# Optimization experiments

Hardware: AMD Instinct MI355X
Metric: run time of the kernel (lower is better)

The kernel has to match this reference:

```python
import jax, jax.numpy as jnp
import numpy as np

E = 3_200_000
D = 16
N = 100_000


def setup_inputs() -> dict:
    key = jax.random.key(0)
    k1, k2 = jax.random.split(key)
    x = jax.random.normal(k1, (E, D), dtype=jnp.float32)
    edge_dst = jax.random.randint(k2, (E,), 0, N, dtype=jnp.int64)
    return {"x": x, "edge_dst": edge_dst, "num_nodes": N}


def reference(x, edge_dst, num_nodes):
    # sum_over_neighbours: scatter-add edge features to destination atoms -> [N, D]
    summed = jax.ops.segment_sum(x, edge_dst, num_segments=num_nodes)
    # number_of_neighbours(include_central_atom=True): per-atom edge count + 1
    counts = jax.ops.segment_sum(
        jnp.ones((x.shape[0],), dtype=x.dtype), edge_dst, num_segments=num_nodes
    ) + jnp.asarray(1.0, dtype=x.dtype)
    # left_aligned_div by sqrt(counts): broadcast counts over trailing feature dims
    return summed / jnp.sqrt(counts)[:, None]
```

## Files before the change

### kernel.cpp

```cpp
#include <hip/hip_runtime.h>

#define DFEAT 16
#define NPB 64
#define NPB_SHIFT 6
#define EB 8192
#define EB_SHIFT 13
#define BIN_THREADS 1024
#define SCAN_BLOCKS 256
#define SCAN_THREADS 256
#define SORT_CAP 4096

__global__ void na_bin_kernel(const int* __restrict__ edge_dst,
                              unsigned short* __restrict__ rank,
                              int* __restrict__ hist,
                              int E, int B, int nblocks) {
    extern __shared__ int h[];
    const int b = blockIdx.x;
    const int t = threadIdx.x;
    for (int i = t; i < B; i += BIN_THREADS) h[i] = 0;
    __syncthreads();
    const int base = b * EB;
    #pragma unroll
    for (int j = 0; j < EB / BIN_THREADS; ++j) {
        int e = base + j * BIN_THREADS + t;
        if (e < E) {
            int k = edge_dst[e] >> NPB_SHIFT;
            int r = atomicAdd(&h[k], 1);
            rank[e] = (unsigned short)r;
        }
    }
    __syncthreads();
    for (int i = t; i < B; i += BIN_THREADS)
        hist[(size_t)i * nblocks + b] = h[i];
}

__global__ void na_scan_partials(const int* __restrict__ data,
                                 int* __restrict__ blockSums, int M) {
    __shared__ int lds[SCAN_THREADS];
    const int b = blockIdx.x, t = threadIdx.x;
    const int chb = (M + SCAN_BLOCKS - 1) / SCAN_BLOCKS;
    const int bbeg = b * chb;
    const int bend = min(bbeg + chb, M);
    const int cht = (chb + SCAN_THREADS - 1) / SCAN_THREADS;
    const int beg = min(bbeg + t * cht, bend);
    const int end = min(beg + cht, bend);
    int s = 0;
    for (int i = beg; i < end; ++i) s += data[i];
    lds[t] = s;
    __syncthreads();
    for (int off = SCAN_THREADS / 2; off > 0; off >>= 1) {
        if (t < off) lds[t] += lds[t + off];
        __syncthreads();
    }
    if (t == 0) blockSums[b] = lds[0];
}

__global__ void na_scan_blocksums(const int* __restrict__ blockSums,
                                  int* __restrict__ blockOffs) {
    __shared__ int lds[SCAN_BLOCKS];
    const int t = threadIdx.x;
    int v = blockSums[t];
    lds[t] = v;
    __syncthreads();
    for (int off = 1; off < SCAN_BLOCKS; off <<= 1) {
        int add = (t >= off) ? lds[t - off] : 0;
        __syncthreads();
        lds[t] += add;
        __syncthreads();
    }
    blockOffs[t] = lds[t] - v;
}

__global__ void na_scan_final(int* __restrict__ data,
                              const int* __restrict__ blockOffs, int M) {
    __shared__ int lds[SCAN_THREADS];
    const int b = blockIdx.x, t = threadIdx.x;
    const int chb = (M + SCAN_BLOCKS - 1) / SCAN_BLOCKS;
    const int bbeg = b * chb;
    const int bend = min(bbeg + chb, M);
    const int cht = (chb + SCAN_THREADS - 1) / SCAN_THREADS;
    const int beg = min(bbeg + t * cht, bend);
    const int end = min(beg + cht, bend);
    int s = 0;
    for (int i = beg; i < end; ++i) s += data[i];
    lds[t] = s;
    __syncthreads();
    for (int off = 1; off < SCAN_THREADS; off <<= 1) {
        int add = (t >= off) ? lds[t - off] : 0;
        __syncthreads();
        lds[t] += add;
        __syncthreads();
    }
    int run = blockOffs[b] + lds[t] - s;
    for (int i = beg; i < end; ++i) {
        int c = data[i];
        data[i] = run;
        run += c;
    }
}

__global__ void na_scatter_bin(const int* __restrict__ edge_dst,
                               const unsigned short* __restrict__ rank,
                               const int* __restrict__ offs,
                               int* __restrict__ binned,
                               int E, int nblocks) {
    int e = blockIdx.x * blockDim.x + threadIdx.x;
    if (e >= E) return;
    int n = edge_dst[e];
    int k = n >> NPB_SHIFT;
    int b = e >> EB_SHIFT;
    int pos = offs[(size_t)k * nblocks + b] + (int)rank[e];
    binned[pos] = ((n & (NPB - 1)) << 22) | e;
}

__global__ __launch_bounds__(256, 4)
void na_sort_gather(const float* __restrict__ x,
                    const int* __restrict__ binned,
                    const int* __restrict__ offs,
                    float* __restrict__ out,
                    int E, int N, int B, int nblocks) {
    __shared__ int buf[SORT_CAP];
    __shared__ int sorted[SORT_CAP];
    __shared__ int cnt[NPB];
    __shared__ int cur[NPB];
    __shared__ int excl[NPB + 1];

    const int k = blockIdx.x;
    const int t = threadIdx.x;

    const int beg = offs[(size_t)k * nblocks];
    const int end = (k + 1 < B) ? offs[(size_t)(k + 1) * nblocks] : E;
    const int sz = end - beg;

    if (t < NPB) { cnt[t] = 0; cur[t] = 0; }
    __syncthreads();

    if (sz <= SORT_CAP) {
        for (int j = t; j < sz; j += 256) {
            int v = binned[beg + j];
            buf[j] = v;
            atomicAdd(&cnt[v >> 22], 1);
        }
        __syncthreads();
        if (t == 0) {
            int run = 0;
            for (int d = 0; d < NPB; ++d) { excl[d] = run; run += cnt[d]; }
            excl[NPB] = run;
        }
        __syncthreads();
        for (int j = t; j < sz; j += 256) {
            int v = buf[j];
            int d = v >> 22;
            int r = atomicAdd(&cur[d], 1);
            sorted[excl[d] + r] = v & 0x3FFFFF;
        }
        __syncthreads();

        const int g = t >> 4;
        const int lane16 = t & 15;
        const int es = lane16 >> 2;
        const int q = lane16 & 3;
        const float4* x4 = reinterpret_cast<const float4*>(x);

        for (int ln = g; ln < NPB; ln += 16) {
            int n = k * NPB + ln;
            if (n >= N) break;
            int lbeg = excl[ln], lend = excl[ln + 1];
            float ax = 0.f, ay = 0.f, az = 0.f, aw = 0.f;

            int i = lbeg + es;
            for (; i + 12 < lend; i += 16) {
                int e0 = sorted[i];
                int e1 = sorted[i + 4];
                int e2 = sorted[i + 8];
                int e3 = sorted[i + 12];
                float4 v0 = x4[(size_t)e0 * 4 + q];
                float4 v1 = x4[(size_t)e1 * 4 + q];
                float4 v2 = x4[(size_t)e2 * 4 + q];
                float4 v3 = x4[(size_t)e3 * 4 + q];
                ax += (v0.x + v1.x) + (v2.x + v3.x);
                ay += (v0.y + v1.y) + (v2.y + v3.y);
                az += (v0.z + v1.z) + (v2.z + v3.z);
                aw += (v0.w + v1.w) + (v2.w + v3.w);
            }
            for (; i < lend; i += 4) {
                int e0 = sorted[i];
                float4 v0 = x4[(size_t)e0 * 4 + q];
                ax += v0.x; ay += v0.y; az += v0.z; aw += v0.w;
            }

            ax += __shfl_xor(ax, 4); ay += __shfl_xor(ay, 4);
            az += __shfl_xor(az, 4); aw += __shfl_xor(aw, 4);
            ax += __shfl_xor(ax, 8); ay += __shfl_xor(ay, 8);
            az += __shfl_xor(az, 8); aw += __shfl_xor(aw, 8);

            float s = rsqrtf((float)(lend - lbeg) + 1.0f);
            if (es == 0) {
                float4 r; r.x = ax * s; r.y = ay * s; r.z = az * s; r.w = aw * s;
                reinterpret_cast<float4*>(out)[(size_t)n * 4 + q] = r;
            }
        }
    } else {
        const int g = t >> 4;
        const int f = t & 15;
        for (int ln = g; ln < NPB; ln += 16) {
            int n = k * NPB + ln;
            if (n >= N) break;
            float acc = 0.0f;
            int deg = 0;
            for (int j = 0; j < sz; ++j) {
                int v = binned[beg + j];
                if ((v >> 22) == ln) {
                    acc += x[(size_t)(v & 0x3FFFFF) * DFEAT + f];
                    ++deg;
                }
            }
            out[(size_t)n * DFEAT + f] = acc * rsqrtf((float)deg + 1.0f);
        }
    }
}

extern "C" void kernel_launch(void* const* d_in, const int* in_sizes, int n_in,
                              void* d_out, int out_size, void* d_ws, size_t ws_size,
                              hipStream_t stream) {
    const float* x        = (const float*)d_in[0];
    const int*   edge_dst = (const int*)d_in[1];
    float*       out      = (float*)d_out;

    const int E = in_sizes[1];
    const int N = out_size / DFEAT;
    const int B = (N + NPB - 1) >> NPB_SHIFT;
    const int nblocks = (E + EB - 1) >> EB_SHIFT;
    const int M = B * nblocks;

    unsigned short* rank = (unsigned short*)d_ws;
    int* binned    = (int*)((char*)d_ws + (((size_t)E * 2 + 3) & ~(size_t)3));
    int* hist      = binned + E;
    int* blockSums = hist + M;
    int* blockOffs = blockSums + SCAN_BLOCKS;

    na_bin_kernel<<<nblocks, BIN_THREADS, B * sizeof(int), stream>>>(
        edge_dst, rank, hist, E, B, nblocks);
    na_scan_partials<<<SCAN_BLOCKS, SCAN_THREADS, 0, stream>>>(hist, blockSums, M);
    na_scan_blocksums<<<1, SCAN_BLOCKS, 0, stream>>>(blockSums, blockOffs);
    na_scan_final<<<SCAN_BLOCKS, SCAN_THREADS, 0, stream>>>(hist, blockOffs, M);
    na_scatter_bin<<<(E + 255) / 256, 256, 0, stream>>>(
        edge_dst, rank, hist, binned, E, nblocks);
    na_sort_gather<<<B, 256, 0, stream>>>(x, binned, hist, out, E, N, B, nblocks);
}
```

Baseline: 125.5 us.

## Drop rank array by recomputing bin positions with LDS atomics in scatter

The histogram kernel no longer writes a per-edge 16-bit rank. Instead the scatter kernel loads each block's scanned offsets into shared memory and takes positions with LDS atomics, which removes the rank write and read traffic. The gather stage now assigns one node per 4-thread group with an 8-way unrolled edge loop and no cross-lane shuffle reduction, and the serial 64-entry prefix sum becomes a wavefront shuffle scan. The edge order within a bin becomes nondeterministic, so floating-point summation order can vary from run to run, and load balance across threads now follows node degree.

```diff
diff --git a/kernel.cpp b/kernel.cpp
--- a/kernel.cpp
+++ b/kernel.cpp
@@ -11,7 +11,6 @@
 #define SORT_CAP 4096
 
 __global__ void na_bin_kernel(const int* __restrict__ edge_dst,
-                              unsigned short* __restrict__ rank,
                               int* __restrict__ hist,
                               int E, int B, int nblocks) {
     extern __shared__ int h[];
@@ -23,11 +22,7 @@
     #pragma unroll
     for (int j = 0; j < EB / BIN_THREADS; ++j) {
         int e = base + j * BIN_THREADS + t;
-        if (e < E) {
-            int k = edge_dst[e] >> NPB_SHIFT;
-            int r = atomicAdd(&h[k], 1);
-            rank[e] = (unsigned short)r;
-        }
+        if (e < E) atomicAdd(&h[edge_dst[e] >> NPB_SHIFT], 1);
     }
     __syncthreads();
     for (int i = t; i < B; i += BIN_THREADS)
@@ -99,18 +94,26 @@
     }
 }
 
-__global__ void na_scatter_bin(const int* __restrict__ edge_dst,
-                               const unsigned short* __restrict__ rank,
-                               const int* __restrict__ offs,
-                               int* __restrict__ binned,
-                               int E, int nblocks) {
-    int e = blockIdx.x * blockDim.x + threadIdx.x;
-    if (e >= E) return;
-    int n = edge_dst[e];
-    int k = n >> NPB_SHIFT;
-    int b = e >> EB_SHIFT;
-    int pos = offs[(size_t)k * nblocks + b] + (int)rank[e];
-    binned[pos] = ((n & (NPB - 1)) << 22) | e;
+__global__ void na_scatter_fused(const int* __restrict__ edge_dst,
+                                 const int* __restrict__ offs,
+                                 int* __restrict__ binned,
+                                 int E, int B, int nblocks) {
+    extern __shared__ int h[];
+    const int b = blockIdx.x;
+    const int t = threadIdx.x;
+    for (int i = t; i < B; i += BIN_THREADS)
+        h[i] = offs[(size_t)i * nblocks + b];
+    __syncthreads();
+    const int base = b * EB;
+    #pragma unroll
+    for (int j = 0; j < EB / BIN_THREADS; ++j) {
+        int e = base + j * BIN_THREADS + t;
+        if (e < E) {
+            int n = edge_dst[e];
+            int pos = atomicAdd(&h[n >> NPB_SHIFT], 1);
+            binned[pos] = ((n & (NPB - 1)) << 22) | e;
+        }
+    }
 }
 
 __global__ __launch_bounds__(256, 4)
@@ -142,10 +145,16 @@
             atomicAdd(&cnt[v >> 22], 1);
         }
         __syncthreads();
-        if (t == 0) {
-            int run = 0;
-            for (int d = 0; d < NPB; ++d) { excl[d] = run; run += cnt[d]; }
-            excl[NPB] = run;
+        if (t < 64) {
+            int v = cnt[t];
+            int inc = v;
+            #pragma unroll
+            for (int d = 1; d < 64; d <<= 1) {
+                int u = __shfl_up(inc, d);
+                if (t >= d) inc += u;
+            }
+            excl[t] = inc - v;
+            if (t == 63) excl[NPB] = inc;
         }
         __syncthreads();
         for (int j = t; j < sz; j += 256) {
@@ -156,66 +165,63 @@
         }
         __syncthreads();
 
-        const int g = t >> 4;
-        const int lane16 = t & 15;
-        const int es = lane16 >> 2;
-        const int q = lane16 & 3;
+        const int ln = t >> 2;
+        const int q = t & 3;
         const float4* x4 = reinterpret_cast<const float4*>(x);
 
-        for (int ln = g; ln < NPB; ln += 16) {
-            int n = k * NPB + ln;
-            if (n >= N) break;
-            int lbeg = excl[ln], lend = excl[ln + 1];
+        const int lbeg = excl[ln], lend = excl[ln + 1];
+        float ax = 0.f, ay = 0.f, az = 0.f, aw = 0.f;
+
+        int i = lbeg;
+        for (; i + 8 <= lend; i += 8) {
+            int e0 = sorted[i + 0], e1 = sorted[i + 1];
+            int e2 = sorted[i + 2], e3 = sorted[i + 3];
+            int e4 = sorted[i + 4], e5 = sorted[i + 5];
+            int e6 = sorted[i + 6], e7 = sorted[i + 7];
+            float4 v0 = x4[(size_t)e0 * 4 + q];
+            float4 v1 = x4[(size_t)e1 * 4 + q];
+            float4 v2 = x4[(size_t)e2 * 4 + q];
+            float4 v3 = x4[(size_t)e3 * 4 + q];
+            float4 v4 = x4[(size_t)e4 * 4 + q];
+            float4 v5 = x4[(size_t)e5 * 4 + q];
+            float4 v6 = x4[(size_t)e6 * 4 + q];
+            float4 v7 = x4[(size_t)e7 * 4 + q];
+            ax += ((v0.x + v1.x) + (v2.x + v3.x)) + ((v4.x + v5.x) + (v6.x + v7.x));
+            ay += ((v0.y + v1.y) + (v2.y + v3.y)) + ((v4.y + v5.y) + (v6.y + v7.y));
+            az += ((v0.z + v1.z) + (v2.z + v3.z)) + ((v4.z + v5.z) + (v6.z + v7.z));
+            aw += ((v0.w + v1.w) + (v2.w + v3.w)) + ((v4.w + v5.w) + (v6.w + v7.w));
+        }
+        for (; i < lend; ++i) {
+            int e0 = sorted[i];
+            float4 v0 = x4[(size_t)e0 * 4 + q];
+            ax += v0.x; ay += v0.y; az += v0.z; aw += v0.w;
+        }
+
+        int n = k * NPB + ln;
+        if (n < N) {
+            float s = rsqrtf((float)(lend - lbeg) + 1.0f);
+            float4 r; r.x = ax * s; r.y = ay * s; r.z = az * s; r.w = aw * s;
+            reinterpret_cast<float4*>(out)[(size_t)n * 4 + q] = r;
+        }
+    } else {
+        const int ln = t >> 2;
+        const int q = t & 3;
+        const float4* x4 = reinterpret_cast<const float4*>(x);
+        int n = k * NPB + ln;
+        if (n < N) {
             float ax = 0.f, ay = 0.f, az = 0.f, aw = 0.f;
-
-            int i = lbeg + es;
-            for (; i + 12 < lend; i += 16) {
-                int e0 = sorted[i];
-                int e1 = sorted[i + 4];
-                int e2 = sorted[i + 8];
-                int e3 = sorted[i + 12];
-                float4 v0 = x4[(size_t)e0 * 4 + q];
-                float4 v1 = x4[(size_t)e1 * 4 + q];
-                float4 v2 = x4[(size_t)e2 * 4 + q];
-                float4 v3 = x4[(size_t)e3 * 4 + q];
-                ax += (v0.x + v1.x) + (v2.x + v3.x);
-                ay += (v0.y + v1.y) + (v2.y + v3.y);
-                az += (v0.z + v1.z) + (v2.z + v3.z);
-                aw += (v0.w + v1.w) + (v2.w + v3.w);
-            }
-            for (; i < lend; i += 4) {
-                int e0 = sorted[i];
-                float4 v0 = x4[(size_t)e0 * 4 + q];
-                ax += v0.x; ay += v0.y; az += v0.z; aw += v0.w;
-            }
-
-            ax += __shfl_xor(ax, 4); ay += __shfl_xor(ay, 4);
-            az += __shfl_xor(az, 4); aw += __shfl_xor(aw, 4);
-            ax += __shfl_xor(ax, 8); ay += __shfl_xor(ay, 8);
-            az += __shfl_xor(az, 8); aw += __shfl_xor(aw, 8);
-
-            float s = rsqrtf((float)(lend - lbeg) + 1.0f);
-            if (es == 0) {
-                float4 r; r.x = ax * s; r.y = ay * s; r.z = az * s; r.w = aw * s;
-                reinterpret_cast<float4*>(out)[(size_t)n * 4 + q] = r;
-            }
-        }
-    } else {
-        const int g = t >> 4;
-        const int f = t & 15;
-        for (int ln = g; ln < NPB; ln += 16) {
-            int n = k * NPB + ln;
-            if (n >= N) break;
-            float acc = 0.0f;
             int deg = 0;
             for (int j = 0; j < sz; ++j) {
                 int v = binned[beg + j];
                 if ((v >> 22) == ln) {
-                    acc += x[(size_t)(v & 0x3FFFFF) * DFEAT + f];
+                    float4 vv = x4[(size_t)(v & 0x3FFFFF) * 4 + q];
+                    ax += vv.x; ay += vv.y; az += vv.z; aw += vv.w;
                     ++deg;
                 }
             }
-            out[(size_t)n * DFEAT + f] = acc * rsqrtf((float)deg + 1.0f);
+            float s = rsqrtf((float)deg + 1.0f);
+            float4 r; r.x = ax * s; r.y = ay * s; r.z = az * s; r.w = aw * s;
+            reinterpret_cast<float4*>(out)[(size_t)n * 4 + q] = r;
         }
     }
 }
@@ -233,18 +239,17 @@
     const int nblocks = (E + EB - 1) >> EB_SHIFT;
     const int M = B * nblocks;
 
-    unsigned short* rank = (unsigned short*)d_ws;
-    int* binned    = (int*)((char*)d_ws + (((size_t)E * 2 + 3) & ~(size_t)3));
+    int* binned    = (int*)d_ws;
     int* hist      = binned + E;
     int* blockSums = hist + M;
     int* blockOffs = blockSums + SCAN_BLOCKS;
 
     na_bin_kernel<<<nblocks, BIN_THREADS, B * sizeof(int), stream>>>(
-        edge_dst, rank, hist, E, B, nblocks);
+        edge_dst, hist, E, B, nblocks);
     na_scan_partials<<<SCAN_BLOCKS, SCAN_THREADS, 0, stream>>>(hist, blockSums, M);
     na_scan_blocksums<<<1, SCAN_BLOCKS, 0, stream>>>(blockSums, blockOffs);
     na_scan_final<<<SCAN_BLOCKS, SCAN_THREADS, 0, stream>>>(hist, blockOffs, M);
-    na_scatter_bin<<<(E + 255) / 256, 256, 0, stream>>>(
-        edge_dst, rank, hist, binned, E, nblocks);
+    na_scatter_fused<<<nblocks, BIN_THREADS, B * sizeof(int), stream>>>(
+        edge_dst, hist, binned, E, B, nblocks);
     na_sort_gather<<<B, 256, 0, stream>>>(x, binned, hist, out, E, N, B, nblocks);
 }
```

Result: slower. 130.7 us (+4.2%).
